# Optimization experiments

Hardware: AMD Instinct MI355X
Metric: run time of the kernel (lower is better)

The kernel has to match this reference:

```python
import jax, jax.numpy as jnp
import numpy as np
import math

N_SAMPLES = 15


def sample_match(P, n_samples=N_SAMPLES):
    """Greedy argmax matching with row/col suppression, vectorized over batch.
    P: [B, N, M] (non-negative softmax scores). Returns (rows, cols): [B, S] int32.
    Matches torch: idx = (P == P.max()).nonzero()[0] -> first (row-major) argmax.
    """
    B, N, M = P.shape
    row_ids = jnp.arange(N)
    col_ids = jnp.arange(M)

    def step(P, _):
        flat_idx = jnp.argmax(P.reshape(B, N * M), axis=1)  # first max, row-major
        row = flat_idx // M  # [B]
        col = flat_idx % M   # [B]
        # suppress chosen row and column: P[row,:]=0 ; P[:,col]=0
        mask = (row_ids[None, :, None] == row[:, None, None]) | (
            col_ids[None, None, :] == col[:, None, None])  # [B,N,M]
        P = jnp.where(mask, jnp.zeros((), P.dtype), P)
        return P, (row, col)

    _, (rows, cols) = jax.lax.scan(step, P, None, length=n_samples)
    return rows.T, cols.T  # [B, S]


def setup_inputs() -> dict:
    key = jax.random.key(0)
    k1, k2, k3, k4 = jax.random.split(key, 4)
    B, D, N = 16, 512, 2048
    return {
        "src_embedding": jax.random.normal(k1, (B, D, N), dtype=jnp.float32),
        "tgt_embedding": jax.random.normal(k2, (B, D, N), dtype=jnp.float32),
        "src": jax.random.normal(k3, (B, N, 3), dtype=jnp.float32),
        "tgt": jax.random.normal(k4, (B, N, 3), dtype=jnp.float32),
    }


def reference(src_embedding, tgt_embedding, src, tgt):
    # input_shape == 'bnc': permute point clouds to [B, 3, N]
    src = jnp.swapaxes(src, 1, 2)
    tgt = jnp.swapaxes(tgt, 1, 2)
    B = src.shape[0]
    d_k = src_embedding.shape[1]

    # scores[b, s, t] = softmax_t( <src_emb[b,:,s], tgt_emb[b,:,t]> / sqrt(d_k) )
    logits = jnp.einsum('bds,bdt->bst', src_embedding, tgt_embedding) / math.sqrt(d_k)
    scores = jax.nn.softmax(logits, axis=2)

    # greedy one-to-one matching on detached scores
    rows, cols = sample_match(jax.lax.stop_gradient(scores))  # [B, S]

    # gather matched points: [B, 3, S]
    topk_src = jnp.take_along_axis(src, rows[:, None, :], axis=2)
    topk_tgt = jnp.take_along_axis(tgt, cols[:, None, :], axis=2)

    src_c = topk_src - topk_src.mean(axis=2, keepdims=True)
    tgt_c = topk_tgt - topk_tgt.mean(axis=2, keepdims=True)
    H = jnp.einsum('bis,bjs->bij', src_c, tgt_c)  # [B, 3, 3]

    u, s, vh = jnp.linalg.svd(H)
    v = jnp.swapaxes(vh, -1, -2)  # torch.svd returns V, jnp returns V^H
    ut = jnp.swapaxes(u, -1, -2)
    r = v @ ut
    det = jnp.linalg.det(r)
    reflect = jnp.array([1.0, 1.0, -1.0], dtype=H.dtype)  # diag(1,1,-1) right-mult
    r_fix = (v * reflect[None, None, :]) @ ut
    R = jnp.where((det < 0)[:, None, None], r_fix, r)  # [B, 3, 3]

    # soft correspondence: src_corr = tgt @ scores^T  -> [B, 3, N_src]
    src_corr = jnp.einsum('bjt,bst->bjs', tgt, scores)
    t = jnp.einsum('bij,bj->bi', -R, src.mean(axis=2)) + src_corr.mean(axis=2)
    return R, t.reshape(B, 3)
```

## Files before the change

### kernel.cpp

```cpp
#include <hip/hip_runtime.h>
#include <hip/hip_fp16.h>
#include <math.h>

typedef unsigned short u16;
typedef __attribute__((ext_vector_type(8))) short bf16x8;
typedef __attribute__((ext_vector_type(4))) float f32x4;

constexpr int B_ = 16;
constexpr int D_ = 512;
constexpr int N_ = 2048;
constexpr int S_ = 15;
constexpr int TOPK = 16;

constexpr int BK  = 32;
constexpr int KP  = 2 * D_;
constexpr int BN7 = 256;
constexpr int SCW4 = 68;
constexpr int SBUF = 24576;

__device__ __forceinline__ void gl_lds16(const void* g, void* s) {
    __builtin_amdgcn_global_load_lds(
        (const __attribute__((address_space(1))) unsigned int*)g,
        (__attribute__((address_space(3))) unsigned int*)s, 16, 0, 0);
}

__device__ __forceinline__ unsigned enc1(float x) {
    x = fminf(x, 448.f);
    unsigned u = __float_as_uint(x);
    if (u < 0x3C800000u) return 0u;
    unsigned r = u + 0x7FFFFu + ((u >> 20) & 1u);
    unsigned f = (r >> 20) - 0x3C0u;
    return f > 0x7Eu ? 0x7Eu : f;
}
__device__ __forceinline__ float dec1(unsigned f) {
    return f ? __uint_as_float((f + 0x3C0u) << 20) : 0.f;
}

__global__ __launch_bounds__(256) void packbf(
    const float* __restrict__ srcE, const float* __restrict__ tgtE,
    u16* __restrict__ srcP, u16* __restrict__ tgtP)
{
    const int t = threadIdx.x;
    const int b = blockIdx.z & 15, sel = blockIdx.z >> 4;
    const float* in = (sel ? tgtE : srcE) + (size_t)b * D_ * N_;
    const int n0 = blockIdx.x * 64, k0 = blockIdx.y * 64;

    __shared__ float T[64][69];

    #pragma unroll
    for (int it = 0; it < 4; it++) {
        int r = it * 16 + (t >> 4);
        int c = (t & 15) * 4;
        float4 v = *(const float4*)&in[(size_t)(k0 + r) * N_ + n0 + c];
        T[r][c + 0] = v.x; T[r][c + 1] = v.y; T[r][c + 2] = v.z; T[r][c + 3] = v.w;
    }
    __syncthreads();

    const int tg = t & 127, kt_i = t >> 7;
    const int panel = n0 >> 7, wb = (n0 & 127) >> 4;
    const int kt = (k0 >> 5) + kt_i;
    char* outA = (char*)srcP;
    char* outB = (char*)tgtP;

    #pragma unroll
    for (int rep = 0; rep < 2; rep++) {
        const int g = rep * 128 + tg;
        const int wi = g >> 6, l = g & 63;
        const int w = wb + wi;
        const int s = (l & 3) ^ ((l >> 3) & 3);
        const int n_loc = wi * 16 + (l >> 2);
        const int kb = kt_i * 32 + s * 8;
        __align__(16) u16 hi[8], lo[8];
        #pragma unroll
        for (int j = 0; j < 8; j++) {
            float x = T[kb + j][n_loc];
            unsigned u = __float_as_uint(x);
            unsigned hr = u + 0x7fff + ((u >> 16) & 1);
            u16 h = (u16)(hr >> 16);
            float hf = __uint_as_float((unsigned)h << 16);
            float xl = x - hf;
            unsigned ul = __float_as_uint(xl);
            unsigned lr = ul + 0x7fff + ((ul >> 16) & 1);
            hi[j] = h; lo[j] = (u16)(lr >> 16);
        }
        if (!sel) {
            size_t base = (((size_t)(b * 16 + panel)) << 18) + ((size_t)kt << 14)
                        + ((size_t)w << 10) + ((size_t)l << 4);
            *(int4*)(outA + base)        = *(int4*)hi;
            *(int4*)(outA + base + 8192) = *(int4*)lo;
        } else {
            size_t base = ((size_t)b << 22) + ((size_t)(panel >> 1) << 19)
                        + ((size_t)kt << 15) + ((size_t)(panel & 1) << 13)
                        + ((size_t)w << 10) + ((size_t)l << 4);
            *(int4*)(outB + base)         = *(int4*)hi;
            *(int4*)(outB + base + 16384) = *(int4*)lo;
        }
    }
}

__global__ __launch_bounds__(512, 2) void gemm7(
    const u16* __restrict__ srcP, const u16* __restrict__ tgtP,
    float* __restrict__ rzbuf, float* __restrict__ topv, int* __restrict__ topc,
    unsigned char* __restrict__ e8)
{
    __shared__ __align__(16) u16 sS[2 * SBUF];
    __shared__ __align__(16) float sC[128 * SCW4];

    const int tid = threadIdx.x;
    const int w = tid >> 6, lane = tid & 63;
    const int wr = w >> 2, wc = w & 3;
    const int sr = lane >> 2, q = lane & 3;
    const int bid = blockIdx.x;
    const int swz = (bid & 7) * 32 + (bid >> 3);
    const int b  = swz >> 4;
    const int s0 = (swz & 15) * 128;
    const float scale = 0.044194173824159216f;
    const int l16 = lane * 16;

    const char* aimg = (const char*)srcP + (((size_t)(b * 16 + (s0 >> 7))) << 18);
    const char* bimg = (const char*)tgtP + ((size_t)b << 22);

    const int aro = (lane & 15) * BK + (((lane >> 4) ^ ((lane >> 1) & 3)) * 8);

    auto stage = [&](int bi, int kt, int ch) {
        u16* base = &sS[bi * SBUF];
        const char* astep = aimg + ((size_t)kt << 14);
        const char* bstep = bimg + ((size_t)ch << 19) + ((size_t)kt << 15);
        #pragma unroll
        for (int j = 0; j < 2; j++)
            gl_lds16(astep + ((w * 2 + j) << 10) + l16, base + (w * 2 + j) * 512);
        #pragma unroll
        for (int j = 0; j < 4; j++)
            gl_lds16(bstep + ((w * 4 + j) << 10) + l16, base + 8192 + (w * 4 + j) * 512);
    };

    float z_loc = 0.f;
    float tv[TOPK]; int tc16[TOPK];
    #pragma unroll
    for (int k = 0; k < TOPK; k++) { tv[k] = -1e30f; tc16[k] = 0x7fffffff; }

    stage(0, 0, 0);

    for (int ch = 0; ch < 8; ch++) {
        const int c0 = ch * BN7;
        f32x4 acc[4][4];
        #pragma unroll
        for (int i = 0; i < 4; i++)
            #pragma unroll
            for (int j = 0; j < 4; j++) acc[i][j] = (f32x4){0.f, 0.f, 0.f, 0.f};

        for (int kt = 0; kt < 16; kt++) {
            __syncthreads();
            if (kt < 15)      stage((kt + 1) & 1, kt + 1, ch);
            else if (ch < 7)  stage(0, 0, ch + 1);
            const u16* base = &sS[(kt & 1) * SBUF];
            bf16x8 ah[4], bh[4], tf[4];
            #pragma unroll
            for (int j = 0; j < 4; j++)
                bh[j] = *(const bf16x8*)&base[8192 + wc * 2048 + j * 512 + aro];
            #pragma unroll
            for (int i = 0; i < 4; i++)
                ah[i] = *(const bf16x8*)&base[wr * 2048 + i * 512 + aro];
            #pragma unroll
            for (int i = 0; i < 4; i++)
                #pragma unroll
                for (int j = 0; j < 4; j++)
                    acc[i][j] = __builtin_amdgcn_mfma_f32_16x16x32_bf16(
                        ah[i], bh[j], acc[i][j], 0, 0, 0);
            #pragma unroll
            for (int i = 0; i < 4; i++)
                tf[i] = *(const bf16x8*)&base[4096 + wr * 2048 + i * 512 + aro];
            #pragma unroll
            for (int i = 0; i < 4; i++)
                #pragma unroll
                for (int j = 0; j < 4; j++)
                    acc[i][j] = __builtin_amdgcn_mfma_f32_16x16x32_bf16(
                        tf[i], bh[j], acc[i][j], 0, 0, 0);
            #pragma unroll
            for (int j = 0; j < 4; j++)
                tf[j] = *(const bf16x8*)&base[16384 + wc * 2048 + j * 512 + aro];
            #pragma unroll
            for (int i = 0; i < 4; i++)
                #pragma unroll
                for (int j = 0; j < 4; j++)
                    acc[i][j] = __builtin_amdgcn_mfma_f32_16x16x32_bf16(
                        ah[i], tf[j], acc[i][j], 0, 0, 0);
        }

        #pragma unroll 1
        for (int h = 0; h < 4; h++) {
            asm volatile("s_waitcnt lgkmcnt(0)" ::: "memory");
            __builtin_amdgcn_s_barrier();
            if (wc == h) {
                #pragma unroll
                for (int i = 0; i < 4; i++)
                    #pragma unroll
                    for (int j = 0; j < 4; j++)
                        #pragma unroll
                        for (int r = 0; r < 4; r++)
                            sC[(wr * 64 + i * 16 + (lane >> 4) * 4 + r) * SCW4
                               + j * 16 + (lane & 15)] = acc[i][j][r] * scale;
            }
            asm volatile("s_waitcnt lgkmcnt(0)" ::: "memory");
            __builtin_amdgcn_s_barrier();
            const float* rowp = &sC[(w * 16 + sr) * SCW4 + q * 16];
            const int cbase = c0 + h * 64 + q * 16;
            unsigned ow0 = 0, ow1 = 0, ow2 = 0, ow3 = 0;
            #pragma unroll
            for (int mi = 0; mi < 4; mi++) {
                float4 v4 = *(const float4*)&rowp[mi * 4];
                const float vv[4] = {v4.x, v4.y, v4.z, v4.w};
                unsigned wb2 = 0;
                #pragma unroll
                for (int e = 0; e < 4; e++) {
                    float v = vv[e];
                    float ex = __expf(v);
                    z_loc += ex;
                    wb2 |= enc1(ex) << (8 * e);
                    if (v > tv[15]) {
                        const int c = cbase + mi * 4 + e;
                        #pragma unroll
                        for (int k = 15; k >= 1; k--) {
                            bool bk  = v > tv[k];
                            bool bk1 = v > tv[k - 1];
                            float sv = bk1 ? tv[k - 1] : v;
                            int   sc = bk1 ? tc16[k - 1] : c;
                            tv[k]   = bk ? sv : tv[k];
                            tc16[k] = bk ? sc : tc16[k];
                        }
                        if (v > tv[0]) { tv[0] = v; tc16[0] = c; }
                    }
                }
                if (mi == 0) ow0 = wb2; else if (mi == 1) ow1 = wb2;
                else if (mi == 2) ow2 = wb2; else ow3 = wb2;
            }
            if (e8) {
                const size_t erow = ((size_t)(b * N_ + s0 + w * 16 + sr)) * N_ + cbase;
                *(uint4*)&e8[erow] = make_uint4(ow0, ow1, ow2, ow3);
            }
        }
    }

    float* sCw = (float*)sS + w * 2112;
    int*   cbw = (int*)sCw;
    float* vbw = sCw + 1024;
    float* zqw = sCw + 2048;
    zqw[lane] = z_loc;
    #pragma unroll
    for (int k = 0; k < TOPK; k++) {
        vbw[lane * 16 + k] = tv[k];
        cbw[lane * 16 + k] = tc16[k];
    }
    if (q == 0) {
        float Z = zqw[lane] + zqw[lane + 1] + zqw[lane + 2] + zqw[lane + 3];
        float lz = logf(Z);
        const int grow = s0 + w * 16 + sr;
        rzbuf[b * N_ + grow] = 1.0f / Z;
        float tmin = -1e30f; int tminslot = 0, tmincol = 0x7fffffff;
        #pragma unroll
        for (int k = 0; k < TOPK; k++) { tv[k] = -1e30f; tc16[k] = 0x7fffffff; }
        for (int qq = 0; qq < 4; qq++) {
            #pragma unroll 1
            for (int k = 0; k < TOPK; k++) {
                float v = vbw[(lane + qq) * 16 + k];
                int c = cbw[(lane + qq) * 16 + k];
                bool ins = (v > tmin) || (v == tmin && c < tmincol);
                if (ins) {
                    #pragma unroll
                    for (int k2 = 0; k2 < TOPK; k2++)
                        if (k2 == tminslot) { tv[k2] = v; tc16[k2] = c; }
                    tmin = tv[0]; tmincol = tc16[0]; tminslot = 0;
                    #pragma unroll
                    for (int k2 = 1; k2 < TOPK; k2++) {
                        bool worse = (tv[k2] < tmin) || (tv[k2] == tmin && tc16[k2] > tmincol);
                        if (worse) { tmin = tv[k2]; tmincol = tc16[k2]; tminslot = k2; }
                    }
                }
            }
        }
        unsigned used = 0;
        size_t rowbase = ((size_t)b * N_ + grow) * TOPK;
        for (int o = 0; o < TOPK; o++) {
            float bvv = -1e31f; int bcc = 0x7fffffff; int bk = 0;
            #pragma unroll
            for (int k = 0; k < TOPK; k++) {
                bool u = (used >> k) & 1u;
                bool better = !u && ((tv[k] > bvv) || (tv[k] == bvv && tc16[k] < bcc));
                if (better) { bvv = tv[k]; bcc = tc16[k]; bk = k; }
            }
            used |= 1u << bk;
            topv[rowbase + o] = bvv - lz;
            topc[rowbase + o] = bcc;
        }
    }
}

__global__ __launch_bounds__(256) void colsum3(
    const unsigned char* __restrict__ e8, const float* __restrict__ rzbuf,
    float* __restrict__ colsum)
{
    const int b = blockIdx.z, s0 = blockIdx.y * 128, t0 = blockIdx.x * 1024;
    __shared__ float srz[128];
    if (threadIdx.x < 128) srz[threadIdx.x] = rzbuf[b * N_ + s0 + threadIdx.x];
    __syncthreads();
    const int t = t0 + threadIdx.x * 4;
    const unsigned char* p = e8 + ((size_t)(b * N_ + s0)) * N_ + t;
    float a0 = 0.f, a1 = 0.f, a2 = 0.f, a3 = 0.f;
    #pragma unroll 4
    for (int s = 0; s < 128; s++) {
        unsigned v = *(const unsigned*)(p + (size_t)s * N_);
        float r = srz[s];
        a0 += dec1(v & 255u) * r;
        a1 += dec1((v >> 8) & 255u) * r;
        a2 += dec1((v >> 16) & 255u) * r;
        a3 += dec1(v >> 24) * r;
    }
    atomicAdd(&colsum[b * N_ + t + 0], a0);
    atomicAdd(&colsum[b * N_ + t + 1], a1);
    atomicAdd(&colsum[b * N_ + t + 2], a2);
    atomicAdd(&colsum[b * N_ + t + 3], a3);
}

__global__ __launch_bounds__(512, 2) void gemm8(
    const u16* __restrict__ srcP, const u16* __restrict__ tgtP,
    const float* __restrict__ rzbuf, float* __restrict__ colsum)
{
    __shared__ __align__(16) u16 sS[2 * SBUF];
    __shared__ float sRZ[128];

    const int tid = threadIdx.x;
    const int w = tid >> 6, lane = tid & 63;
    const int wr = w >> 2, wc = w & 3;
    const int bid = blockIdx.x;
    const int swz = (bid & 7) * 32 + (bid >> 3);
    const int b  = swz >> 4;
    const int s0 = (swz & 15) * 128;
    const float scale = 0.044194173824159216f;
    const int l16 = lane * 16;

    const char* aimg = (const char*)srcP + (((size_t)(b * 16 + (s0 >> 7))) << 18);
    const char* bimg = (const char*)tgtP + ((size_t)b << 22);
    const int aro = (lane & 15) * BK + (((lane >> 4) ^ ((lane >> 1) & 3)) * 8);

    if (tid < 128) sRZ[tid] = rzbuf[b * N_ + s0 + tid];

    auto stage = [&](int bi, int kt, int ch) {
        u16* base = &sS[bi * SBUF];
        const char* astep = aimg + ((size_t)kt << 14);
        const char* bstep = bimg + ((size_t)ch << 19) + ((size_t)kt << 15);
        #pragma unroll
        for (int j = 0; j < 2; j++)
            gl_lds16(astep + ((w * 2 + j) << 10) + l16, base + (w * 2 + j) * 512);
        #pragma unroll
        for (int j = 0; j < 4; j++)
            gl_lds16(bstep + ((w * 4 + j) << 10) + l16, base + 8192 + (w * 4 + j) * 512);
    };

    stage(0, 0, 0);

    for (int ch = 0; ch < 8; ch++) {
        const int c0 = ch * BN7;
        f32x4 acc[4][4];
        #pragma unroll
        for (int i = 0; i < 4; i++)
            #pragma unroll
            for (int j = 0; j < 4; j++) acc[i][j] = (f32x4){0.f, 0.f, 0.f, 0.f};

        for (int kt = 0; kt < 16; kt++) {
            __syncthreads();
            if (kt < 15)      stage((kt + 1) & 1, kt + 1, ch);
            else if (ch < 7)  stage(0, 0, ch + 1);
            const u16* base = &sS[(kt & 1) * SBUF];
            bf16x8 ah[4], bh[4], tf[4];
            #pragma unroll
            for (int j = 0; j < 4; j++)
                bh[j] = *(const bf16x8*)&base[8192 + wc * 2048 + j * 512 + aro];
            #pragma unroll
            for (int i = 0; i < 4; i++)
                ah[i] = *(const bf16x8*)&base[wr * 2048 + i * 512 + aro];
            #pragma unroll
            for (int i = 0; i < 4; i++)
                #pragma unroll
                for (int j = 0; j < 4; j++)
                    acc[i][j] = __builtin_amdgcn_mfma_f32_16x16x32_bf16(
                        ah[i], bh[j], acc[i][j], 0, 0, 0);
            #pragma unroll
            for (int i = 0; i < 4; i++)
                tf[i] = *(const bf16x8*)&base[4096 + wr * 2048 + i * 512 + aro];
            #pragma unroll
            for (int i = 0; i < 4; i++)
                #pragma unroll
                for (int j = 0; j < 4; j++)
                    acc[i][j] = __builtin_amdgcn_mfma_f32_16x16x32_bf16(
                        tf[i], bh[j], acc[i][j], 0, 0, 0);
            #pragma unroll
            for (int j = 0; j < 4; j++)
                tf[j] = *(const bf16x8*)&base[16384 + wc * 2048 + j * 512 + aro];
            #pragma unroll
            for (int i = 0; i < 4; i++)
                #pragma unroll
                for (int j = 0; j < 4; j++)
                    acc[i][j] = __builtin_amdgcn_mfma_f32_16x16x32_bf16(
                        ah[i], tf[j], acc[i][j], 0, 0, 0);
        }

        #pragma unroll
        for (int j = 0; j < 4; j++) {
            float s = 0.f;
            #pragma unroll
            for (int i = 0; i < 4; i++)
                #pragma unroll
                for (int r = 0; r < 4; r++)
                    s += __expf(acc[i][j][r] * scale)
                         * sRZ[wr * 64 + i * 16 + (lane >> 4) * 4 + r];
            s += __shfl_xor(s, 16);
            s += __shfl_xor(s, 32);
            if (lane < 16)
                atomicAdd(&colsum[b * N_ + c0 + wc * 64 + j * 16 + lane], s);
        }
    }
}

__global__ __launch_bounds__(256) void match2(
    const float* __restrict__ topv, const int* __restrict__ topc,
    int* __restrict__ mrow, int* __restrict__ mcol)
{
    const int b = blockIdx.x, tid = threadIdx.x;
    __shared__ float bv[N_];
    __shared__ int bc[N_];
    __shared__ int sup[16];
    __shared__ float rv[256];
    __shared__ int rr[256];

    for (int r = tid; r < N_; r += 256) {
        bv[r] = topv[((size_t)b * N_ + r) * TOPK];
        bc[r] = topc[((size_t)b * N_ + r) * TOPK];
    }
    __syncthreads();

    for (int it = 0; it < S_; it++) {
        float mv = -1e30f; int mr = 0x7fffffff;
        #pragma unroll
        for (int j = 0; j < 8; j++) {
            int r = tid + j * 256;
            float v = bv[r];
            if (v > mv) { mv = v; mr = r; }
        }
        rv[tid] = mv; rr[tid] = mr;
        __syncthreads();
        for (int off = 128; off; off >>= 1) {
            if (tid < off) {
                float v2 = rv[tid + off];
                if (v2 > rv[tid] || (v2 == rv[tid] && rr[tid + off] < rr[tid])) {
                    rv[tid] = v2; rr[tid] = rr[tid + off];
                }
            }
            __syncthreads();
        }
        if (tid == 0) {
            int R = rr[0]; int C = bc[R];
            mrow[b * S_ + it] = R; mcol[b * S_ + it] = C;
            sup[it] = C;
            bv[R] = -1e30f;
        }
        __syncthreads();
        const int C = sup[it];
        for (int r = tid; r < N_; r += 256) {
            if (bc[r] == C && bv[r] > -1e29f) {
                float nv = -1e30f; int nc = 0x7fffffff;
                const float* tvp = &topv[((size_t)b * N_ + r) * TOPK];
                const int* tcp = &topc[((size_t)b * N_ + r) * TOPK];
                for (int k = 0; k < TOPK; k++) {
                    int c2 = tcp[k];
                    bool bad = false;
                    for (int qq = 0; qq <= it; qq++) bad = bad || (sup[qq] == c2);
                    if (!bad) { nv = tvp[k]; nc = c2; break; }
                }
                bv[r] = nv; bc[r] = nc;
            }
        }
        __syncthreads();
    }
}

__global__ void finish_kernel(const float* __restrict__ src,
                              const float* __restrict__ tgt,
                              const float* __restrict__ colsum,
                              const int* __restrict__ mrow,
                              const int* __restrict__ mcol,
                              float* __restrict__ out)
{
    const int b = blockIdx.x;
    const int tid = threadIdx.x;
    __shared__ float red[256];
    __shared__ float res[6];

    float ls[3] = {0, 0, 0}, lc[3] = {0, 0, 0};
    for (int n = tid; n < N_; n += 256) {
        float cs = colsum[b * N_ + n];
        #pragma unroll
        for (int j = 0; j < 3; j++) {
            ls[j] += src[(size_t)(b * N_ + n) * 3 + j];
            lc[j] += tgt[(size_t)(b * N_ + n) * 3 + j] * cs;
        }
    }
    for (int j = 0; j < 6; j++) {
        red[tid] = (j < 3) ? ls[j] : lc[j - 3];
        __syncthreads();
        for (int off = 128; off; off >>= 1) {
            if (tid < off) red[tid] += red[tid + off];
            __syncthreads();
        }
        if (tid == 0) res[j] = red[0] / (float)N_;
        __syncthreads();
    }

    if (tid == 0) {
        double ps[S_][3], pt[S_][3];
        double ms[3] = {0, 0, 0}, mt[3] = {0, 0, 0};
        for (int s = 0; s < S_; s++) {
            int r = mrow[b * S_ + s], c = mcol[b * S_ + s];
            for (int j = 0; j < 3; j++) {
                ps[s][j] = (double)src[(size_t)(b * N_ + r) * 3 + j];
                pt[s][j] = (double)tgt[(size_t)(b * N_ + c) * 3 + j];
                ms[j] += ps[s][j]; mt[j] += pt[s][j];
            }
        }
        for (int j = 0; j < 3; j++) { ms[j] /= S_; mt[j] /= S_; }
        double H[3][3] = {{0,0,0},{0,0,0},{0,0,0}};
        for (int s = 0; s < S_; s++)
            for (int i = 0; i < 3; i++)
                for (int j = 0; j < 3; j++)
                    H[i][j] += (ps[s][i] - ms[i]) * (pt[s][j] - mt[j]);

        double A[3][3], Vv[3][3] = {{1,0,0},{0,1,0},{0,0,1}};
        for (int i = 0; i < 3; i++)
            for (int j = 0; j < 3; j++) {
                double acc = 0;
                for (int k = 0; k < 3; k++) acc += H[k][i] * H[k][j];
                A[i][j] = acc;
            }
        for (int sweep = 0; sweep < 30; sweep++) {
            double off = fabs(A[0][1]) + fabs(A[0][2]) + fabs(A[1][2]);
            if (off < 1e-30) break;
            for (int pair = 0; pair < 3; pair++) {
                int p = (pair == 2) ? 1 : 0;
                int q = (pair == 0) ? 1 : 2;
                double apq = A[p][q];
                if (fabs(apq) < 1e-300) continue;
                double theta = (A[q][q] - A[p][p]) / (2.0 * apq);
                double tt = ((theta >= 0) ? 1.0 : -1.0) / (fabs(theta) + sqrt(theta * theta + 1.0));
                double cc = 1.0 / sqrt(tt * tt + 1.0);
                double ssn = tt * cc;
                for (int k = 0; k < 3; k++) {
                    double akp = A[k][p], akq = A[k][q];
                    A[k][p] = cc * akp - ssn * akq;
                    A[k][q] = ssn * akp + cc * akq;
                }
                for (int k = 0; k < 3; k++) {
                    double apk = A[p][k], aqk = A[q][k];
                    A[p][k] = cc * apk - ssn * aqk;
                    A[q][k] = ssn * apk + cc * aqk;
                }
                for (int k = 0; k < 3; k++) {
                    double vkp = Vv[k][p], vkq = Vv[k][q];
                    Vv[k][p] = cc * vkp - ssn * vkq;
                    Vv[k][q] = ssn * vkp + cc * vkq;
                }
            }
        }
        double wv[3] = {A[0][0], A[1][1], A[2][2]};
        for (int a = 0; a < 2; a++)
            for (int b2 = a + 1; b2 < 3; b2++)
                if (wv[b2] > wv[a]) {
                    double tw = wv[a]; wv[a] = wv[b2]; wv[b2] = tw;
                    for (int k = 0; k < 3; k++) {
                        double tv_ = Vv[k][a]; Vv[k][a] = Vv[k][b2]; Vv[k][b2] = tv_;
                    }
                }
        double U[3][3];
        for (int k = 0; k < 3; k++) {
            double u[3], nrm = 0;
            for (int i = 0; i < 3; i++) {
                double acc = 0;
                for (int j = 0; j < 3; j++) acc += H[i][j] * Vv[j][k];
                u[i] = acc; nrm += acc * acc;
            }
            nrm = sqrt(nrm);
            if (nrm < 1e-300) nrm = 1e-300;
            for (int i = 0; i < 3; i++) U[i][k] = u[i] / nrm;
        }
        double r[3][3];
        for (int i = 0; i < 3; i++)
            for (int j = 0; j < 3; j++) {
                double acc = 0;
                for (int k = 0; k < 3; k++) acc += Vv[i][k] * U[j][k];
                r[i][j] = acc;
            }
        double det = r[0][0] * (r[1][1] * r[2][2] - r[1][2] * r[2][1])
                   - r[0][1] * (r[1][0] * r[2][2] - r[1][2] * r[2][0])
                   + r[0][2] * (r[1][0] * r[2][1] - r[1][1] * r[2][0]);
        if (det < 0.0) {
            for (int i = 0; i < 3; i++)
                for (int j = 0; j < 3; j++)
                    r[i][j] -= 2.0 * Vv[i][2] * U[j][2];
        }
        double smean[3] = {(double)res[0], (double)res[1], (double)res[2]};
        double cmean[3] = {(double)res[3], (double)res[4], (double)res[5]};
        for (int i = 0; i < 3; i++)
            for (int j = 0; j < 3; j++)
                out[b * 9 + i * 3 + j] = (float)r[i][j];
        for (int i = 0; i < 3; i++) {
            double acc = cmean[i];
            for (int j = 0; j < 3; j++) acc -= r[i][j] * smean[j];
            out[B_ * 9 + b * 3 + i] = (float)acc;
        }
    }
}

extern "C" void kernel_launch(void* const* d_in, const int* in_sizes, int n_in,
                              void* d_out, int out_size, void* d_ws, size_t ws_size,
                              hipStream_t stream)
{
    const float* srcE = (const float*)d_in[0];
    const float* tgtE = (const float*)d_in[1];
    const float* src  = (const float*)d_in[2];
    const float* tgt  = (const float*)d_in[3];
    float* out = (float*)d_out;
    char* ws = (char*)d_ws;

    const size_t szP  = (size_t)B_ * N_ * KP * sizeof(u16);
    const size_t szE8 = (size_t)B_ * N_ * N_;
    const size_t szStats = (size_t)B_ * N_ * sizeof(float)
                         + (size_t)B_ * N_ * TOPK * sizeof(float)
                         + (size_t)B_ * N_ * TOPK * sizeof(int)
                         + (size_t)B_ * N_ * sizeof(float)
                         + 2048;
    const bool fat = ws_size >= 2 * szP + szE8 + szStats;

    u16* srcP = (u16*)ws;
    u16* tgtP = (u16*)(ws + szP);
    unsigned char* e8 = fat ? (unsigned char*)(ws + 2 * szP) : nullptr;
    size_t off = 2 * szP + (fat ? szE8 : 0);
    float* rzbuf  = (float*)(ws + off); off += (size_t)B_ * N_ * sizeof(float);
    float* topv   = (float*)(ws + off); off += (size_t)B_ * N_ * TOPK * sizeof(float);
    int*   topc   = (int*)(ws + off);   off += (size_t)B_ * N_ * TOPK * sizeof(int);
    float* colsum = (float*)(ws + off); off += (size_t)B_ * N_ * sizeof(float);
    int*   mrow   = (int*)(ws + off);   off += 1024;
    int*   mcol   = (int*)(ws + off);

    hipMemsetAsync(colsum, 0, (size_t)B_ * N_ * sizeof(float), stream);

    packbf<<<dim3(N_ / 64, D_ / 64, 2 * B_), 256, 0, stream>>>(srcE, tgtE, srcP, tgtP);
    gemm7<<<dim3(256), 512, 0, stream>>>(srcP, tgtP, rzbuf, topv, topc, e8);
    if (fat)
        colsum3<<<dim3(2, 16, 16), 256, 0, stream>>>(e8, rzbuf, colsum);
    else
        gemm8<<<dim3(256), 512, 0, stream>>>(srcP, tgtP, rzbuf, colsum);
    match2<<<B_, 256, 0, stream>>>(topv, topc, mrow, mcol);
    finish_kernel<<<B_, 256, 0, stream>>>(src, tgt, colsum, mrow, mcol, out);
}
```

Baseline: 722.5 us.

## Shrink gemm7 tiles to 64x128 and double the grid for more occupancy

Rewrites gemm7 to compute 64-row by 128-column output tiles with a 2x2 MFMA accumulator per wave instead of 128x256 with 4x4, and launches 512 blocks instead of 256 with launch bounds raised to 4 blocks per CU. Each thread now handles 4 columns per pass rather than 16. The final top-k merge becomes an 8-way merge of already sorted per-lane lists instead of the insertion-and-select scheme. The goal is better latency hiding and fewer idle CUs on a 256-block grid, at the cost of less operand reuse per block and more global/LDS traffic for the B operand.

```diff
diff --git a/kernel.cpp b/kernel.cpp
--- a/kernel.cpp
+++ b/kernel.cpp
@@ -14,9 +14,8 @@
 
 constexpr int BK  = 32;
 constexpr int KP  = 2 * D_;
-constexpr int BN7 = 256;
-constexpr int SCW4 = 68;
-constexpr int SBUF = 24576;
+constexpr int SB7 = 12288;
+constexpr int SCW = 36;
 
 __device__ __forceinline__ void gl_lds16(const void* g, void* s) {
     __builtin_amdgcn_global_load_lds(
@@ -98,24 +97,24 @@
     }
 }
 
-__global__ __launch_bounds__(512, 2) void gemm7(
+__global__ __launch_bounds__(512, 4) void gemm7(
     const u16* __restrict__ srcP, const u16* __restrict__ tgtP,
     float* __restrict__ rzbuf, float* __restrict__ topv, int* __restrict__ topc,
     unsigned char* __restrict__ e8)
 {
-    __shared__ __align__(16) u16 sS[2 * SBUF];
-    __shared__ __align__(16) float sC[128 * SCW4];
+    __shared__ __align__(16) u16 sS[2 * SB7];
+    __shared__ __align__(16) float sC[64 * SCW];
 
     const int tid = threadIdx.x;
     const int w = tid >> 6, lane = tid & 63;
     const int wr = w >> 2, wc = w & 3;
-    const int sr = lane >> 2, q = lane & 3;
     const int bid = blockIdx.x;
-    const int swz = (bid & 7) * 32 + (bid >> 3);
-    const int b  = swz >> 4;
-    const int s0 = (swz & 15) * 128;
+    const int swz = (bid & 7) * 64 + (bid >> 3);
+    const int b  = swz >> 5;
+    const int s0 = (swz & 31) * 64;
     const float scale = 0.044194173824159216f;
     const int l16 = lane * 16;
+    const int wb = (s0 & 127) >> 4;
 
     const char* aimg = (const char*)srcP + (((size_t)(b * 16 + (s0 >> 7))) << 18);
     const char* bimg = (const char*)tgtP + ((size_t)b << 22);
@@ -123,15 +122,15 @@
     const int aro = (lane & 15) * BK + (((lane >> 4) ^ ((lane >> 1) & 3)) * 8);
 
     auto stage = [&](int bi, int kt, int ch) {
-        u16* base = &sS[bi * SBUF];
+        u16* base = &sS[bi * SB7];
         const char* astep = aimg + ((size_t)kt << 14);
-        const char* bstep = bimg + ((size_t)ch << 19) + ((size_t)kt << 15);
-        #pragma unroll
-        for (int j = 0; j < 2; j++)
-            gl_lds16(astep + ((w * 2 + j) << 10) + l16, base + (w * 2 + j) * 512);
-        #pragma unroll
-        for (int j = 0; j < 4; j++)
-            gl_lds16(bstep + ((w * 4 + j) << 10) + l16, base + 8192 + (w * 4 + j) * 512);
+        const char* bstep = bimg + ((size_t)(ch >> 1) << 19) + ((size_t)kt << 15)
+                          + ((size_t)(ch & 1) << 13);
+        const int sec = w >> 2;
+        gl_lds16(astep + (sec << 13) + ((wb + (w & 3)) << 10) + l16,
+                 base + sec * 2048 + (w & 3) * 512);
+        gl_lds16(bstep + (w << 10) + l16,          base + 4096 + w * 512);
+        gl_lds16(bstep + 16384 + (w << 10) + l16,  base + 8192 + w * 512);
     };
 
     float z_loc = 0.f;
@@ -141,48 +140,47 @@
 
     stage(0, 0, 0);
 
-    for (int ch = 0; ch < 8; ch++) {
-        const int c0 = ch * BN7;
-        f32x4 acc[4][4];
-        #pragma unroll
-        for (int i = 0; i < 4; i++)
-            #pragma unroll
-            for (int j = 0; j < 4; j++) acc[i][j] = (f32x4){0.f, 0.f, 0.f, 0.f};
+    for (int ch = 0; ch < 16; ch++) {
+        f32x4 acc[2][2];
+        #pragma unroll
+        for (int i = 0; i < 2; i++)
+            #pragma unroll
+            for (int j = 0; j < 2; j++) acc[i][j] = (f32x4){0.f, 0.f, 0.f, 0.f};
 
         for (int kt = 0; kt < 16; kt++) {
             __syncthreads();
             if (kt < 15)      stage((kt + 1) & 1, kt + 1, ch);
-            else if (ch < 7)  stage(0, 0, ch + 1);
-            const u16* base = &sS[(kt & 1) * SBUF];
-            bf16x8 ah[4], bh[4], tf[4];
-            #pragma unroll
-            for (int j = 0; j < 4; j++)
-                bh[j] = *(const bf16x8*)&base[8192 + wc * 2048 + j * 512 + aro];
-            #pragma unroll
-            for (int i = 0; i < 4; i++)
-                ah[i] = *(const bf16x8*)&base[wr * 2048 + i * 512 + aro];
-            #pragma unroll
-            for (int i = 0; i < 4; i++)
-                #pragma unroll
-                for (int j = 0; j < 4; j++)
+            else if (ch < 15) stage(0, 0, ch + 1);
+            const u16* base = &sS[(kt & 1) * SB7];
+            bf16x8 ah[2], bh[2], tf[2];
+            #pragma unroll
+            for (int j = 0; j < 2; j++)
+                bh[j] = *(const bf16x8*)&base[4096 + (wc * 2 + j) * 512 + aro];
+            #pragma unroll
+            for (int i = 0; i < 2; i++)
+                ah[i] = *(const bf16x8*)&base[(wr * 2 + i) * 512 + aro];
+            #pragma unroll
+            for (int i = 0; i < 2; i++)
+                #pragma unroll
+                for (int j = 0; j < 2; j++)
                     acc[i][j] = __builtin_amdgcn_mfma_f32_16x16x32_bf16(
                         ah[i], bh[j], acc[i][j], 0, 0, 0);
             #pragma unroll
-            for (int i = 0; i < 4; i++)
-                tf[i] = *(const bf16x8*)&base[4096 + wr * 2048 + i * 512 + aro];
-            #pragma unroll
-            for (int i = 0; i < 4; i++)
-                #pragma unroll
-                for (int j = 0; j < 4; j++)
+            for (int i = 0; i < 2; i++)
+                tf[i] = *(const bf16x8*)&base[2048 + (wr * 2 + i) * 512 + aro];
+            #pragma unroll
+            for (int i = 0; i < 2; i++)
+                #pragma unroll
+                for (int j = 0; j < 2; j++)
                     acc[i][j] = __builtin_amdgcn_mfma_f32_16x16x32_bf16(
                         tf[i], bh[j], acc[i][j], 0, 0, 0);
             #pragma unroll
-            for (int j = 0; j < 4; j++)
-                tf[j] = *(const bf16x8*)&base[16384 + wc * 2048 + j * 512 + aro];
-            #pragma unroll
-            for (int i = 0; i < 4; i++)
-                #pragma unroll
-                for (int j = 0; j < 4; j++)
+            for (int j = 0; j < 2; j++)
+                tf[j] = *(const bf16x8*)&base[8192 + (wc * 2 + j) * 512 + aro];
+            #pragma unroll
+            for (int i = 0; i < 2; i++)
+                #pragma unroll
+                for (int j = 0; j < 2; j++)
                     acc[i][j] = __builtin_amdgcn_mfma_f32_16x16x32_bf16(
                         ah[i], tf[j], acc[i][j], 0, 0, 0);
         }
@@ -193,104 +191,90 @@
             __builtin_amdgcn_s_barrier();
             if (wc == h) {
                 #pragma unroll
-                for (int i = 0; i < 4; i++)
+                for (int i = 0; i < 2; i++)
                     #pragma unroll
-                    for (int j = 0; j < 4; j++)
+                    for (int j = 0; j < 2; j++)
                         #pragma unroll
                         for (int r = 0; r < 4; r++)
-                            sC[(wr * 64 + i * 16 + (lane >> 4) * 4 + r) * SCW4
+                            sC[(wr * 32 + i * 16 + (lane >> 4) * 4 + r) * SCW
                                + j * 16 + (lane & 15)] = acc[i][j][r] * scale;
             }
             asm volatile("s_waitcnt lgkmcnt(0)" ::: "memory");
             __builtin_amdgcn_s_barrier();
-            const float* rowp = &sC[(w * 16 + sr) * SCW4 + q * 16];
-            const int cbase = c0 + h * 64 + q * 16;
-            unsigned ow0 = 0, ow1 = 0, ow2 = 0, ow3 = 0;
-            #pragma unroll
-            for (int mi = 0; mi < 4; mi++) {
-                float4 v4 = *(const float4*)&rowp[mi * 4];
-                const float vv[4] = {v4.x, v4.y, v4.z, v4.w};
-                unsigned wb2 = 0;
-                #pragma unroll
-                for (int e = 0; e < 4; e++) {
-                    float v = vv[e];
-                    float ex = __expf(v);
-                    z_loc += ex;
-                    wb2 |= enc1(ex) << (8 * e);
-                    if (v > tv[15]) {
-                        const int c = cbase + mi * 4 + e;
-                        #pragma unroll
-                        for (int k = 15; k >= 1; k--) {
-                            bool bk  = v > tv[k];
-                            bool bk1 = v > tv[k - 1];
-                            float sv = bk1 ? tv[k - 1] : v;
-                            int   sc = bk1 ? tc16[k - 1] : c;
-                            tv[k]   = bk ? sv : tv[k];
-                            tc16[k] = bk ? sc : tc16[k];
-                        }
-                        if (v > tv[0]) { tv[0] = v; tc16[0] = c; }
+            const int row = w * 8 + (lane >> 3);
+            float4 v4 = *(const float4*)&sC[row * SCW + (lane & 7) * 4];
+            const float vv[4] = {v4.x, v4.y, v4.z, v4.w};
+            const int cbase = ch * 128 + h * 32 + (lane & 7) * 4;
+            unsigned wb2 = 0;
+            #pragma unroll
+            for (int e = 0; e < 4; e++) {
+                float v = vv[e];
+                float ex = __expf(v);
+                z_loc += ex;
+                wb2 |= enc1(ex) << (8 * e);
+                if (v > tv[15]) {
+                    const int c = cbase + e;
+                    #pragma unroll
+                    for (int k = 15; k >= 1; k--) {
+                        bool bk  = v > tv[k];
+                        bool bk1 = v > tv[k - 1];
+                        float sv = bk1 ? tv[k - 1] : v;
+                        int   sc = bk1 ? tc16[k - 1] : c;
+                        tv[k]   = bk ? sv : tv[k];
+                        tc16[k] = bk ? sc : tc16[k];
                     }
+                    if (v > tv[0]) { tv[0] = v; tc16[0] = c; }
                 }
-                if (mi == 0) ow0 = wb2; else if (mi == 1) ow1 = wb2;
-                else if (mi == 2) ow2 = wb2; else ow3 = wb2;
             }
             if (e8) {
-                const size_t erow = ((size_t)(b * N_ + s0 + w * 16 + sr)) * N_ + cbase;
-                *(uint4*)&e8[erow] = make_uint4(ow0, ow1, ow2, ow3);
-            }
-        }
-    }
-
-    float* sCw = (float*)sS + w * 2112;
-    int*   cbw = (int*)sCw;
-    float* vbw = sCw + 1024;
-    float* zqw = sCw + 2048;
-    zqw[lane] = z_loc;
+                const size_t erow = ((size_t)(b * N_ + s0 + row)) * N_ + cbase;
+                *(unsigned*)&e8[erow] = wb2;
+            }
+        }
+    }
+
+    float Z = z_loc;
+    Z += __shfl_xor(Z, 1); Z += __shfl_xor(Z, 2); Z += __shfl_xor(Z, 4);
+    float* vbw = (float*)((char*)sS + w * 6144);
+    u16*   cbw = (u16*)((char*)sS + w * 6144 + 4096);
+    __syncthreads();
     #pragma unroll
     for (int k = 0; k < TOPK; k++) {
         vbw[lane * 16 + k] = tv[k];
-        cbw[lane * 16 + k] = tc16[k];
-    }
-    if (q == 0) {
-        float Z = zqw[lane] + zqw[lane + 1] + zqw[lane + 2] + zqw[lane + 3];
+        cbw[lane * 16 + k] = (u16)tc16[k];
+    }
+    __syncthreads();
+    if ((lane & 7) == 0) {
+        const int grow = s0 + w * 8 + (lane >> 3);
         float lz = logf(Z);
-        const int grow = s0 + w * 16 + sr;
         rzbuf[b * N_ + grow] = 1.0f / Z;
-        float tmin = -1e30f; int tminslot = 0, tmincol = 0x7fffffff;
-        #pragma unroll
-        for (int k = 0; k < TOPK; k++) { tv[k] = -1e30f; tc16[k] = 0x7fffffff; }
-        for (int qq = 0; qq < 4; qq++) {
-            #pragma unroll 1
-            for (int k = 0; k < TOPK; k++) {
-                float v = vbw[(lane + qq) * 16 + k];
-                int c = cbw[(lane + qq) * 16 + k];
-                bool ins = (v > tmin) || (v == tmin && c < tmincol);
-                if (ins) {
-                    #pragma unroll
-                    for (int k2 = 0; k2 < TOPK; k2++)
-                        if (k2 == tminslot) { tv[k2] = v; tc16[k2] = c; }
-                    tmin = tv[0]; tmincol = tc16[0]; tminslot = 0;
-                    #pragma unroll
-                    for (int k2 = 1; k2 < TOPK; k2++) {
-                        bool worse = (tv[k2] < tmin) || (tv[k2] == tmin && tc16[k2] > tmincol);
-                        if (worse) { tmin = tv[k2]; tmincol = tc16[k2]; tminslot = k2; }
-                    }
-                }
-            }
-        }
-        unsigned used = 0;
+        float hv[8]; int hc[8]; int hix[8];
+        #pragma unroll
+        for (int m = 0; m < 8; m++) {
+            hv[m] = vbw[(lane + m) * 16];
+            hc[m] = cbw[(lane + m) * 16];
+            hix[m] = 1;
+        }
         size_t rowbase = ((size_t)b * N_ + grow) * TOPK;
         for (int o = 0; o < TOPK; o++) {
-            float bvv = -1e31f; int bcc = 0x7fffffff; int bk = 0;
-            #pragma unroll
-            for (int k = 0; k < TOPK; k++) {
-                bool u = (used >> k) & 1u;
-                bool better = !u && ((tv[k] > bvv) || (tv[k] == bvv && tc16[k] < bcc));
-                if (better) { bvv = tv[k]; bcc = tc16[k]; bk = k; }
-            }
-            used |= 1u << bk;
-            topv[rowbase + o] = bvv - lz;
-            topc[rowbase + o] = bcc;
+            float bv = hv[0]; int bc = hc[0]; int bm = 0;
+            #pragma unroll
+            for (int m = 1; m < 8; m++) {
+                bool better = (hv[m] > bv) || (hv[m] == bv && hc[m] < bc);
+                if (better) { bv = hv[m]; bc = hc[m]; bm = m; }
+            }
+            topv[rowbase + o] = bv - lz;
+            topc[rowbase + o] = bc;
+            int ni = 16;
+            #pragma unroll
+            for (int m = 0; m < 8; m++) if (m == bm) ni = hix[m];
+            int rdi = ni < 15 ? ni : 15;
+            float nv = vbw[(lane + bm) * 16 + rdi];
+            int   nc = cbw[(lane + bm) * 16 + rdi];
+            if (ni > 15) nv = -1e30f;
+            #pragma unroll
+            for (int m = 0; m < 8; m++)
+                if (m == bm) { hv[m] = nv; hc[m] = nc; hix[m] = ni + 1; }
         }
     }
 }
@@ -325,7 +309,7 @@
     const u16* __restrict__ srcP, const u16* __restrict__ tgtP,
     const float* __restrict__ rzbuf, float* __restrict__ colsum)
 {
-    __shared__ __align__(16) u16 sS[2 * SBUF];
+    __shared__ __align__(16) u16 sS[2 * 24576];
     __shared__ float sRZ[128];
 
     const int tid = threadIdx.x;
@@ -345,7 +329,7 @@
     if (tid < 128) sRZ[tid] = rzbuf[b * N_ + s0 + tid];
 
     auto stage = [&](int bi, int kt, int ch) {
-        u16* base = &sS[bi * SBUF];
+        u16* base = &sS[bi * 24576];
         const char* astep = aimg + ((size_t)kt << 14);
         const char* bstep = bimg + ((size_t)ch << 19) + ((size_t)kt << 15);
         #pragma unroll
@@ -359,7 +343,7 @@
     stage(0, 0, 0);
 
     for (int ch = 0; ch < 8; ch++) {
-        const int c0 = ch * BN7;
+        const int c0 = ch * 256;
         f32x4 acc[4][4];
         #pragma unroll
         for (int i = 0; i < 4; i++)
@@ -370,7 +354,7 @@
             __syncthreads();
             if (kt < 15)      stage((kt + 1) & 1, kt + 1, ch);
             else if (ch < 7)  stage(0, 0, ch + 1);
-            const u16* base = &sS[(kt & 1) * SBUF];
+            const u16* base = &sS[(kt & 1) * 24576];
             bf16x8 ah[4], bh[4], tf[4];
             #pragma unroll
             for (int j = 0; j < 4; j++)
@@ -652,7 +636,7 @@
     hipMemsetAsync(colsum, 0, (size_t)B_ * N_ * sizeof(float), stream);
 
     packbf<<<dim3(N_ / 64, D_ / 64, 2 * B_), 256, 0, stream>>>(srcE, tgtE, srcP, tgtP);
-    gemm7<<<dim3(256), 512, 0, stream>>>(srcP, tgtP, rzbuf, topv, topc, e8);
+    gemm7<<<dim3(512), 512, 0, stream>>>(srcP, tgtP, rzbuf, topv, topc, e8);
     if (fat)
         colsum3<<<dim3(2, 16, 16), 256, 0, stream>>>(e8, rzbuf, colsum);
     else
```

New measurement: 634.0 us. 12.3% less time.
